# Kernel optimization log

Hardware: AMD Instinct MI355X
Metric: run time of the kernel (lower is better)

The kernel has to match this reference:

```python
import jax, jax.numpy as jnp
import numpy as np

T, N, H, G = 4, 100000, 128, 1024
LN2 = float(np.log(2.0))
EPS = 1e-5


def ssp(x):
    # shifted softplus: softplus(x) - softplus(0)
    return jax.nn.softplus(x) - LN2


def layernorm(x, g, b):
    m = jnp.mean(x, axis=-1, keepdims=True)
    v = jnp.var(x, axis=-1, keepdims=True)
    return (x - m) * jax.lax.rsqrt(v + EPS) * g + b


def mlp3(x, Ws, bs, gs, bts):
    # 3 stacked Linear -> LayerNorm -> SSP stages
    for i in range(3):
        x = ssp(layernorm(x @ Ws[i] + bs[i], gs[i], bts[i]))
    return x


def setup_inputs() -> dict:
    key = jax.random.key(0)
    ks = jax.random.split(key, 8)
    s = 1.0 / np.sqrt(H)
    batch = jnp.sort((jnp.arange(N, dtype=jnp.int64) * G) // N).astype(jnp.int32)
    return {
        "x_proc": jax.random.normal(ks[0], (T, N, H), jnp.float32),
        "x_enc": jax.random.normal(ks[1], (N, H), jnp.float32),
        "batch": batch,
        "pW": jax.random.normal(ks[2], (3, H, H), jnp.float32) * s,
        "pb": jnp.zeros((3, H), jnp.float32),
        "pg": jnp.ones((3, H), jnp.float32),
        "pbt": jnp.zeros((3, H), jnp.float32),
        "eW": jax.random.normal(ks[3], (3, H, H), jnp.float32) * s,
        "eb": jnp.zeros((3, H), jnp.float32),
        "eg": jnp.ones((3, H), jnp.float32),
        "ebt": jnp.zeros((3, H), jnp.float32),
        "wp": jax.random.normal(ks[4], (H, 1), jnp.float32) * s,
        "bp": jnp.zeros((1,), jnp.float32),
        "we": jax.random.normal(ks[5], (H, 1), jnp.float32) * s,
        "be": jnp.zeros((1,), jnp.float32),
    }


def reference(x_proc, x_enc, batch, pW, pb, pg, pbt, eW, eb, eg, ebt, wp, bp, we, be):
    h_proc = mlp3(x_proc, pW, pb, pg, pbt)          # [T, N, H]
    h_enc = mlp3(x_enc, eW, eb, eg, ebt)            # [N, H]
    seg = lambda z: jax.ops.segment_sum(z, batch, num_segments=G)
    pooled_proc = jax.vmap(seg)(h_proc)             # [T, G, H]
    pooled_enc = seg(h_enc)                         # [G, H]
    target = pooled_proc @ wp + bp + (pooled_enc @ we + be)[None]  # [T, G, 1]
    return target.reshape(-1, G)                    # [T, G]
```

## Files before the change

kernel.cpp:

```cpp
#include <hip/hip_runtime.h>
#include <hip/hip_bf16.h>

typedef unsigned short u16;
typedef unsigned int u32;
typedef __bf16 bf16x8 __attribute__((ext_vector_type(8)));
typedef float f32x16 __attribute__((ext_vector_type(16)));
typedef float f32x4 __attribute__((ext_vector_type(4)));
typedef u32 u32x4 __attribute__((ext_vector_type(4)));

#define NN 100000
#define NPROC_BLOCKS 3125
#define NENC_BLOCKS 782
#define LN2F 0.69314718055994530942f
#define LOG2EF 1.44269504088896340736f
#define CSTRIDE 1284

__device__ __forceinline__ u16 f2bf(float f) {
  u32 u = __float_as_uint(f);
  u32 r = u + 0x7fffu + ((u >> 16) & 1u);
  return (u16)(r >> 16);
}

__device__ __forceinline__ u32 pk2(float a, float b) {
  float2 f2; f2.x = a; f2.y = b;
  __hip_bfloat162 h = __float22bfloat162_rn(f2);
  u32 r;
  __builtin_memcpy(&r, &h, 4);
  return r;
}

__device__ __forceinline__ float l2p1e(float xp) {
  return __builtin_amdgcn_logf(1.0f + __builtin_amdgcn_exp2f(xp));
}

__global__ void prep_kernel(const float* __restrict__ pW, const float* __restrict__ eW,
                            const float* __restrict__ pb, const float* __restrict__ pg,
                            const float* __restrict__ pbt,
                            const float* __restrict__ eb, const float* __restrict__ eg,
                            const float* __restrict__ ebt,
                            const float* __restrict__ wp, const float* __restrict__ we,
                            const float* __restrict__ bp, const float* __restrict__ be,
                            u16* __restrict__ wt, float* __restrict__ cprep,
                            float* __restrict__ out) {
  int bx = blockIdx.x;
  int t = threadIdx.x;
  if (bx < 384) {
    int idx = bx * 256 + t;
    int m = idx >> 14;
    int within = idx & 16383;
    int r = within >> 7;
    int c = within & 127;
    int k = (((c >> 3) ^ (r & 15)) << 3) | (c & 7);
    const float* src = (m < 3) ? pW : eW;
    int ms = (m < 3) ? m : m - 3;
    float w = src[ms * 16384 + k * 128 + r];
    if (ms >= 1) w *= LN2F;
    wt[idx] = f2bf(w);
    if (idx < 4096) out[idx] = bp[0] + be[0];
  } else {
    int net = bx - 384;
    const float* W  = net ? eW : pW;
    const float* b  = net ? eb : pb;
    const float* g  = net ? eg : pg;
    const float* bt = net ? ebt : pbt;
    const float* wv = net ? we : wp;
    float* cp = cprep + net * CSTRIDE;
    if (t < 128) {
      int j = t;
      #pragma unroll
      for (int s = 0; s < 3; ++s) {
        float bb = b[s * 128 + j];
        if (s >= 1) {
          float cs = 0.f;
          #pragma unroll 8
          for (int k = 0; k < 128; ++k) cs += W[s * 16384 + k * 128 + j];
          bb -= LN2F * cs;
        }
        cp[(s * 3 + 0) * 128 + j] = bb;
        cp[(s * 3 + 1) * 128 + j] = g[s * 128 + j] * LOG2EF;
        cp[(s * 3 + 2) * 128 + j] = bt[s * 128 + j] * LOG2EF;
      }
      cp[9 * 128 + j] = LN2F * wv[j];
    }
    if (t == 0) {
      float ssum = 0.f;
      #pragma unroll 8
      for (int j = 0; j < 128; ++j) ssum += wv[j];
      cp[1280] = -LN2F * ssum;
    }
  }
}

__global__ __launch_bounds__(256, 3)
void mlp_kernel(const float* __restrict__ x_proc, const float* __restrict__ x_enc,
                const u16* __restrict__ wt, const float* __restrict__ cprep,
                const int* __restrict__ batch, float* __restrict__ out) {
  __shared__ __align__(16) unsigned char wbuf[32768];
  __shared__ f32x4 cball[10][32];
  __shared__ float c0s;

  const bool is_proc = blockIdx.x < NPROC_BLOCKS;
  const int bid2 = is_proc ? blockIdx.x : blockIdx.x - NPROC_BLOCKS;
  const float* x = is_proc ? x_proc : x_enc;
  const unsigned char* wgb = (const unsigned char*)(is_proc ? wt : wt + 49152);
  const float* cp = cprep + (is_proc ? 0 : CSTRIDE);
  const int nrows = is_proc ? 400000 : 100000;

  const int tid = threadIdx.x;
  const int lane = tid & 63;
  const int wid = tid >> 6;
  const int l31 = lane & 31;
  const u32 hi = (u32)(lane >> 5);
  const int brow = bid2 * 128;

  for (int i = tid; i < 320; i += 256)
    ((f32x4*)cball)[i] = *(const f32x4*)(cp + i * 4);
  if (tid == 0) c0s = cp[1280];

  u32x4 wcp[8];
  #pragma unroll
  for (int i = 0; i < 8; ++i)
    wcp[i] = *(const u32x4*)(wgb + i * 4096 + tid * 16);

  const int rloc = wid * 32 + l31;
  const int grow = brow + rloc;
  const float* xr = x + (size_t)((grow < nrows) ? grow : (nrows - 1)) * 128 + (int)hi * 8;
  bf16x8 bfr[8];
  #pragma unroll
  for (int ks = 0; ks < 8; ++ks) {
    f32x4 a0 = *(const f32x4*)(xr + ks * 16);
    f32x4 a1 = *(const f32x4*)(xr + ks * 16 + 4);
    u32x4 tq;
    tq.x = pk2(a0[0], a0[1]);
    tq.y = pk2(a0[2], a0[3]);
    tq.z = pk2(a1[0], a1[1]);
    tq.w = pk2(a1[2], a1[3]);
    bfr[ks] = __builtin_bit_cast(bf16x8, tq);
  }

  float pfin = 0.0f;

  #pragma unroll
  for (int s = 0; s < 3; ++s) {
    #pragma unroll
    for (int i = 0; i < 8; ++i)
      *(u32x4*)(wbuf + i * 4096 + tid * 16) = wcp[i];
    __syncthreads();

    f32x16 acc[4];
    #pragma unroll
    for (int jf = 0; jf < 4; ++jf)
      #pragma unroll
      for (int q = 0; q < 4; ++q) {
        f32x4 b4 = cball[s * 3 + 0][jf * 8 + 2 * q + (int)hi];
        acc[jf][4 * q + 0] = b4[0];
        acc[jf][4 * q + 1] = b4[1];
        acc[jf][4 * q + 2] = b4[2];
        acc[jf][4 * q + 3] = b4[3];
      }

    #pragma unroll
    for (int ks = 0; ks < 8; ++ks)
      #pragma unroll
      for (int jf = 0; jf < 4; ++jf) {
        int rr = jf * 32 + l31;
        const bf16x8 afrag = *(const bf16x8*)(const void*)(
            wbuf + rr * 256 + (((2 * ks + (int)hi) ^ (l31 & 15)) << 4));
        acc[jf] = __builtin_amdgcn_mfma_f32_32x32x16_bf16(afrag, bfr[ks], acc[jf], 0, 0, 0);
      }

    if (s < 2) {
      #pragma unroll
      for (int i = 0; i < 8; ++i)
        wcp[i] = *(const u32x4*)(wgb + (s + 1) * 32768 + i * 4096 + tid * 16);
      __syncthreads();
    }

    float s1 = 0.f, s2 = 0.f;
    #pragma unroll
    for (int jf = 0; jf < 4; ++jf) {
      float p1 = 0.f, p2 = 0.f;
      #pragma unroll
      for (int e = 0; e < 16; ++e) {
        float v = acc[jf][e];
        p1 += v;
        p2 = __builtin_fmaf(v, v, p2);
      }
      s1 += p1; s2 += p2;
    }
    s1 += __shfl_xor(s1, 32, 64);
    s2 += __shfl_xor(s2, 32, 64);
    float mean = s1 * 0.0078125f;
    float var = s2 * 0.0078125f - mean * mean;
    float rstd = rsqrtf(var + 1e-5f);
    float nmr = -mean * rstd;

    if (s < 2) {
      #pragma unroll
      for (int ks = 0; ks < 8; ++ks) {
        int jf = ks >> 1, q0 = (ks & 1) << 1;
        uint2 wq[2];
        #pragma unroll
        for (int qq = 0; qq < 2; ++qq) {
          int q = q0 + qq;
          f32x4 g4 = cball[s * 3 + 1][jf * 8 + 2 * q + (int)hi];
          f32x4 t4 = cball[s * 3 + 2][jf * 8 + 2 * q + (int)hi];
          float r0 = l2p1e((acc[jf][4 * q + 0] * rstd + nmr) * g4[0] + t4[0]);
          float r1 = l2p1e((acc[jf][4 * q + 1] * rstd + nmr) * g4[1] + t4[1]);
          float r2 = l2p1e((acc[jf][4 * q + 2] * rstd + nmr) * g4[2] + t4[2]);
          float r3 = l2p1e((acc[jf][4 * q + 3] * rstd + nmr) * g4[3] + t4[3]);
          wq[qq].x = pk2(r0, r1);
          wq[qq].y = pk2(r2, r3);
        }
        u32 sx = hi ? wq[0].x : wq[1].x;
        u32 sy = hi ? wq[0].y : wq[1].y;
        u32 rx = (u32)__shfl_xor((int)sx, 32, 64);
        u32 ry = (u32)__shfl_xor((int)sy, 32, 64);
        u32x4 tq;
        tq.x = hi ? rx : wq[0].x;
        tq.y = hi ? ry : wq[0].y;
        tq.z = hi ? wq[1].x : rx;
        tq.w = hi ? wq[1].y : ry;
        bfr[ks] = __builtin_bit_cast(bf16x8, tq);
      }
    } else {
      float p = 0.f;
      #pragma unroll
      for (int jf = 0; jf < 4; ++jf)
        #pragma unroll
        for (int q = 0; q < 4; ++q) {
          f32x4 g4 = cball[7][jf * 8 + 2 * q + (int)hi];
          f32x4 t4 = cball[8][jf * 8 + 2 * q + (int)hi];
          f32x4 w4 = cball[9][jf * 8 + 2 * q + (int)hi];
          #pragma unroll
          for (int e = 0; e < 4; ++e) {
            float v = l2p1e((acc[jf][4 * q + e] * rstd + nmr) * g4[e] + t4[e]);
            p = __builtin_fmaf(v, w4[e], p);
          }
        }
      pfin = p;
    }
  }

  pfin += __shfl_xor(pfin, 32, 64);
  if (grow < nrows) {
    pfin += c0s;
    int cell;
    if (is_proc) {
      int tt = grow / NN;
      cell = tt * 1024 + batch[grow - tt * NN];
    } else {
      cell = batch[grow];
    }
    int ca = __shfl(cell, 0, 32);
    int cz = __shfl(cell, 31, 32);
    if (ca == cz) {
      float r = pfin;
      #pragma unroll
      for (int off = 1; off < 32; off <<= 1) r += __shfl_xor(r, off, 64);
      if (hi == 0) {
        if (is_proc) {
          if (l31 == 0) atomicAdd(out + ca, r);
        } else {
          if (l31 < 4) atomicAdd(out + l31 * 1024 + ca, r);
        }
      }
    } else if (hi == 0) {
      if (is_proc) {
        atomicAdd(out + cell, pfin);
      } else {
        #pragma unroll
        for (int t2 = 0; t2 < 4; ++t2) atomicAdd(out + t2 * 1024 + cell, pfin);
      }
    }
  }
}

extern "C" void kernel_launch(void* const* d_in, const int* in_sizes, int n_in,
                              void* d_out, int out_size, void* d_ws, size_t ws_size,
                              hipStream_t stream) {
  const float* x_proc = (const float*)d_in[0];
  const float* x_enc  = (const float*)d_in[1];
  const int*   batch  = (const int*)d_in[2];
  const float* pW  = (const float*)d_in[3];
  const float* pb  = (const float*)d_in[4];
  const float* pg  = (const float*)d_in[5];
  const float* pbt = (const float*)d_in[6];
  const float* eW  = (const float*)d_in[7];
  const float* eb  = (const float*)d_in[8];
  const float* eg  = (const float*)d_in[9];
  const float* ebt = (const float*)d_in[10];
  const float* wp  = (const float*)d_in[11];
  const float* bp  = (const float*)d_in[12];
  const float* we  = (const float*)d_in[13];
  const float* be  = (const float*)d_in[14];

  float* out = (float*)d_out;
  u16* wt_ws = (u16*)d_ws;
  float* cprep = (float*)((char*)d_ws + 196608);

  prep_kernel<<<386, 256, 0, stream>>>(pW, eW, pb, pg, pbt, eb, eg, ebt,
                                       wp, we, bp, be, wt_ws, cprep, out);
  mlp_kernel<<<NPROC_BLOCKS + NENC_BLOCKS, 256, 0, stream>>>(
      x_proc, x_enc, wt_ws, cprep, batch, out);
}
```

Before: 160.4 us.

## Read MFMA weight fragments directly from global memory instead of LDS staging

The prep kernel now writes the bf16 weights in a layout where each lane's four jf fragments for a given k-step sit next to each other. The MLP kernel drops the 32KB LDS weight buffer, its staging copies and the per-stage barriers, and loads A fragments straight from global memory, relying on L1/L2 to serve the 96KB of weights shared by all blocks. This frees LDS and removes synchronisation, which may raise occupancy. In exchange, every wave issues global loads inside the MFMA loop, with higher latency than LDS reads.

Result: slower. 192.6 us (+20.1%).

```diff
diff --git a/kernel.cpp b/kernel.cpp
--- a/kernel.cpp
+++ b/kernel.cpp
@@ -48,9 +48,12 @@
     int idx = bx * 256 + t;
     int m = idx >> 14;
     int within = idx & 16383;
-    int r = within >> 7;
-    int c = within & 127;
-    int k = (((c >> 3) ^ (r & 15)) << 3) | (c & 7);
+    int rl  = within >> 9;
+    int swz = (within >> 5) & 15;
+    int jf  = (within >> 3) & 3;
+    int e   = within & 7;
+    int r = jf * 32 + rl;
+    int k = ((swz ^ (rl & 15)) << 3) | e;
     const float* src = (m < 3) ? pW : eW;
     int ms = (m < 3) ? m : m - 3;
     float w = src[ms * 16384 + k * 128 + r];
@@ -95,7 +98,6 @@
 void mlp_kernel(const float* __restrict__ x_proc, const float* __restrict__ x_enc,
                 const u16* __restrict__ wt, const float* __restrict__ cprep,
                 const int* __restrict__ batch, float* __restrict__ out) {
-  __shared__ __align__(16) unsigned char wbuf[32768];
   __shared__ f32x4 cball[10][32];
   __shared__ float c0s;
 
@@ -116,16 +118,12 @@
   for (int i = tid; i < 320; i += 256)
     ((f32x4*)cball)[i] = *(const f32x4*)(cp + i * 4);
   if (tid == 0) c0s = cp[1280];
-
-  u32x4 wcp[8];
-  #pragma unroll
-  for (int i = 0; i < 8; ++i)
-    wcp[i] = *(const u32x4*)(wgb + i * 4096 + tid * 16);
+  __syncthreads();
 
   const int rloc = wid * 32 + l31;
   const int grow = brow + rloc;
   const float* xr = x + (size_t)((grow < nrows) ? grow : (nrows - 1)) * 128 + (int)hi * 8;
-  bf16x8 bfr[8];
+  bf16x8 bc[8];
   #pragma unroll
   for (int ks = 0; ks < 8; ++ks) {
     f32x4 a0 = *(const f32x4*)(xr + ks * 16);
@@ -135,17 +133,19 @@
     tq.y = pk2(a0[2], a0[3]);
     tq.z = pk2(a1[0], a1[1]);
     tq.w = pk2(a1[2], a1[3]);
-    bfr[ks] = __builtin_bit_cast(bf16x8, tq);
-  }
+    bc[ks] = __builtin_bit_cast(bf16x8, tq);
+  }
+
+  u32 voff[8];
+  #pragma unroll
+  for (int ks = 0; ks < 8; ++ks)
+    voff[ks] = (u32)(l31 * 1024 + (((2 * ks + (int)hi) ^ (l31 & 15)) << 6));
 
   float pfin = 0.0f;
 
   #pragma unroll
   for (int s = 0; s < 3; ++s) {
-    #pragma unroll
-    for (int i = 0; i < 8; ++i)
-      *(u32x4*)(wbuf + i * 4096 + tid * 16) = wcp[i];
-    __syncthreads();
+    const unsigned char* wsb = wgb + s * 32768;
 
     f32x16 acc[4];
     #pragma unroll
@@ -160,20 +160,13 @@
       }
 
     #pragma unroll
-    for (int ks = 0; ks < 8; ++ks)
+    for (int ks = 0; ks < 8; ++ks) {
+      const unsigned char* fp = wsb + voff[ks];
       #pragma unroll
       for (int jf = 0; jf < 4; ++jf) {
-        int rr = jf * 32 + l31;
-        const bf16x8 afrag = *(const bf16x8*)(const void*)(
-            wbuf + rr * 256 + (((2 * ks + (int)hi) ^ (l31 & 15)) << 4));
-        acc[jf] = __builtin_amdgcn_mfma_f32_32x32x16_bf16(afrag, bfr[ks], acc[jf], 0, 0, 0);
-      }
-
-    if (s < 2) {
-      #pragma unroll
-      for (int i = 0; i < 8; ++i)
-        wcp[i] = *(const u32x4*)(wgb + (s + 1) * 32768 + i * 4096 + tid * 16);
-      __syncthreads();
+        const bf16x8 afrag = *(const bf16x8*)(const void*)(fp + jf * 16);
+        acc[jf] = __builtin_amdgcn_mfma_f32_32x32x16_bf16(afrag, bc[ks], acc[jf], 0, 0, 0);
+      }
     }
 
     float s1 = 0.f, s2 = 0.f;
@@ -221,7 +214,7 @@
         tq.y = hi ? ry : wq[0].y;
         tq.z = hi ? wq[1].x : rx;
         tq.w = hi ? wq[1].y : ry;
-        bfr[ks] = __builtin_bit_cast(bf16x8, tq);
+        bc[ks] = __builtin_bit_cast(bf16x8, tq);
       }
     } else {
       float p = 0.f;
```
